# Kernel optimization log

Measured on AMD Instinct MI355X. Metric: run time of the kernel, lower is better.

Reference implementation:

```python
import jax, jax.numpy as jnp
import numpy as np

N_NODES = 10000
N_EDGES = 640000
IN_FEAT = 128
OUT_FEAT = 256


def setup_inputs() -> dict:
    key = jax.random.key(0)
    k_h, k_src, k_dst, k_w, k_b = jax.random.split(key, 5)
    h = jax.random.normal(k_h, (N_NODES, IN_FEAT), dtype=jnp.float32)
    src = jax.random.randint(k_src, (N_EDGES,), 0, N_NODES, dtype=jnp.int64)
    dst = jax.random.randint(k_dst, (N_EDGES,), 0, N_NODES, dtype=jnp.int64)
    W = jax.random.normal(k_w, (2 * IN_FEAT, OUT_FEAT), dtype=jnp.float32) * 0.05
    b = jax.random.normal(k_b, (OUT_FEAT,), dtype=jnp.float32) * 0.05
    return {"h": h, "src": src, "dst": dst, "W": W, "b": b}


def reference(h, src, dst, W, b):
    # Message passing: copy_u('h') then mean-reduce over incoming edges (by dst).
    msgs = h[src]                                   # [E, in_feat] gather
    summed = jax.ops.segment_sum(msgs, dst, num_segments=N_NODES)   # [N, in_feat]
    deg = jax.ops.segment_sum(jnp.ones((src.shape[0],), h.dtype), dst,
                              num_segments=N_NODES)                 # [N]
    h_N = jnp.where(deg[:, None] > 0, summed / jnp.maximum(deg, 1.0)[:, None], 0.0)
    # Concat self + neighbor mean, then dense linear.
    h_total = jnp.concatenate([h, h_N], axis=1)     # [N, 2*in_feat]
    return h_total @ W + b                          # [N, out_feat]
```

## Files before the change

### kernel.cpp

```cpp
#include <hip/hip_runtime.h>
#include <hip/hip_bf16.h>

#define NN 10000
#define NE 640000
#define SB 256
#define EPB 2500
#define NR 625
#define CW 32
#define CE 31
#define CONVB 512

typedef __attribute__((ext_vector_type(8))) short bf16x8;
typedef __attribute__((ext_vector_type(4))) float f32x4;

__device__ __forceinline__ unsigned packbf(float x, float y) {
  __hip_bfloat16 a = __float2bfloat16(x);
  __hip_bfloat16 c = __float2bfloat16(y);
  unsigned short ua = __builtin_bit_cast(unsigned short, a);
  unsigned short uc = __builtin_bit_cast(unsigned short, c);
  return (unsigned)ua | ((unsigned)uc << 16);
}
__device__ __forceinline__ float blo(unsigned u) { return __uint_as_float(u << 16); }
__device__ __forceinline__ float bhi(unsigned u) { return __uint_as_float(u & 0xffff0000u); }

__global__ __launch_bounds__(256) void kA_scatter_conv(
    const float* __restrict__ h, const int* __restrict__ src,
    const int* __restrict__ dst, const float* __restrict__ W,
    unsigned* __restrict__ gbuf, unsigned* __restrict__ hb32,
    unsigned* __restrict__ wb32) {
  int t = threadIdx.x;
  int blk = blockIdx.x;
  if (blk < SB) {
    __shared__ int lc[NR];
    for (int i = t; i < NR; i += 256) lc[i] = 0;
    __syncthreads();
    int base = blk * EPB;
    for (int e = t; e < EPB; e += 256) {
      unsigned d = (unsigned)dst[base + e] & 0x3fffu;
      unsigned sv = (unsigned)src[base + e] & 0x3fffu;
      int range = (int)(d >> 4);
      if (range >= NR) range = NR - 1;
      int r = atomicAdd(&lc[range], 1);
      if (r < CE)
        gbuf[((size_t)range * SB + blk) * CW + 1 + r] = ((d & 15u) << 14) | sv;
    }
    __syncthreads();
    for (int i = t; i < NR; i += 256)
      gbuf[((size_t)i * SB + blk) * CW] = (unsigned)lc[i];
  } else {
    int tid = (blk - SB) * 256 + t;
    const float2* h2 = (const float2*)h;
    for (int j = tid; j < NN * 64; j += CONVB * 256) {
      float2 v = h2[j];
      hb32[j] = packbf(v.x, v.y);
    }
    if (tid < 32768) {
      float2 v = ((const float2*)W)[tid];
      wb32[tid] = packbf(v.x, v.y);
    }
  }
}

__global__ __launch_bounds__(256) void k2_agg_gemm(
    const float* __restrict__ h, const unsigned* __restrict__ gbuf,
    const unsigned* __restrict__ hb32, const unsigned* __restrict__ wb32,
    const float* __restrict__ bias, float* __restrict__ out) {
  __shared__ __align__(16) unsigned short As[16][264];
  __shared__ unsigned short cbuf[16][128];
  __shared__ int lcnt[16];
  int t = threadIdx.x;
  int bm = blockIdx.x;

  if (t < 16) lcnt[t] = 0;

#pragma unroll
  for (int i = 0; i < 2; i++) {
    int q = t + i * 256;
    int row = q >> 5, c4 = q & 31;
    float4 v = *(const float4*)(h + (size_t)(bm * 16 + row) * 128 + c4 * 4);
    uint2 p;
    p.x = packbf(v.x, v.y);
    p.y = packbf(v.z, v.w);
    *(uint2*)(&As[row][c4 * 4]) = p;
  }
  __syncthreads();

  {
    const unsigned* chunk = gbuf + ((size_t)bm * SB + t) * CW;
    int c = (int)(chunk[0] & 0x3fu);
    int kk = c < CE ? c : CE;
    for (int j = 0; j < kk; j++) {
      unsigned v = chunk[1 + j];
      int dstlo = (int)(v >> 14) & 15;
      unsigned sv = v & 0x3fffu;
      int pos = atomicAdd(&lcnt[dstlo], 1);
      if (pos < 128) cbuf[dstlo][pos] = (unsigned short)sv;
    }
  }
  __syncthreads();

  int w = t >> 6, l = t & 63;
#pragma unroll
  for (int i = 0; i < 4; i++) {
    int row = w * 4 + i;
    int deg = lcnt[row];
    int n = deg < 128 ? deg : 128;
    float a0 = 0.f, a1 = 0.f;
    int e = 0;
    for (; e + 7 < n; e += 8) {
      int s0 = cbuf[row][e], s1 = cbuf[row][e + 1], s2 = cbuf[row][e + 2],
          s3 = cbuf[row][e + 3], s4 = cbuf[row][e + 4], s5 = cbuf[row][e + 5],
          s6 = cbuf[row][e + 6], s7 = cbuf[row][e + 7];
      unsigned u0 = hb32[s0 * 64 + l], u1 = hb32[s1 * 64 + l];
      unsigned u2 = hb32[s2 * 64 + l], u3 = hb32[s3 * 64 + l];
      unsigned u4 = hb32[s4 * 64 + l], u5 = hb32[s5 * 64 + l];
      unsigned u6 = hb32[s6 * 64 + l], u7 = hb32[s7 * 64 + l];
      a0 += (blo(u0) + blo(u1)) + (blo(u2) + blo(u3)) +
            ((blo(u4) + blo(u5)) + (blo(u6) + blo(u7)));
      a1 += (bhi(u0) + bhi(u1)) + (bhi(u2) + bhi(u3)) +
            ((bhi(u4) + bhi(u5)) + (bhi(u6) + bhi(u7)));
    }
    for (; e < n; e++) {
      unsigned u = hb32[cbuf[row][e] * 64 + l];
      a0 += blo(u);
      a1 += bhi(u);
    }
    float inv = (deg > 0) ? 1.f / (float)deg : 0.f;
    ((unsigned*)&As[row][128])[l] = packbf(a0 * inv, a1 * inv);
  }
  __syncthreads();

  int lm = l & 15, kb = l >> 4;
  const unsigned short* Wb = (const unsigned short*)wb32;
#pragma unroll
  for (int bn = 0; bn < 4; bn++) {
    int col = bn * 64 + w * 16 + lm;
    bf16x8 bfr[8];
#pragma unroll
    for (int ks = 0; ks < 8; ks++) {
#pragma unroll
      for (int j = 0; j < 8; j++) {
        bfr[ks][j] = (short)Wb[(ks * 32 + kb * 8 + j) * 256 + col];
      }
    }
    f32x4 acc = (f32x4){0.f, 0.f, 0.f, 0.f};
#pragma unroll
    for (int ks = 0; ks < 8; ks++) {
      uint4 araw = *(const uint4*)(&As[lm][ks * 32 + kb * 8]);
      bf16x8 af = __builtin_bit_cast(bf16x8, araw);
      acc = __builtin_amdgcn_mfma_f32_16x16x32_bf16(af, bfr[ks], acc, 0, 0, 0);
    }
    float biasf = bias[col];
#pragma unroll
    for (int reg = 0; reg < 4; reg++) {
      int m = bm * 16 + kb * 4 + reg;
      out[(size_t)m * 256 + col] = acc[reg] + biasf;
    }
  }
}

extern "C" void kernel_launch(void* const* d_in, const int* in_sizes, int n_in,
                              void* d_out, int out_size, void* d_ws, size_t ws_size,
                              hipStream_t stream) {
  const float* h = (const float*)d_in[0];
  const int* src = (const int*)d_in[1];
  const int* dst = (const int*)d_in[2];
  const float* W = (const float*)d_in[3];
  const float* b = (const float*)d_in[4];
  float* out = (float*)d_out;

  char* ws = (char*)d_ws;
  unsigned* gbuf = (unsigned*)(ws + 0);
  unsigned* hb32 = (unsigned*)(ws + 20480000);
  unsigned* wb32 = (unsigned*)(ws + 24674304);

  kA_scatter_conv<<<SB + CONVB, 256, 0, stream>>>(h, src, dst, W, gbuf, hb32, wb32);
  k2_agg_gemm<<<NR, 256, 0, stream>>>(h, gbuf, hb32, wb32, b, out);
}
```

Measured before the change: 106.6 us.

## Prepack W in MFMA fragment order, vectorize neighbor gather, pad edge lists

The scatter kernel now uses 250 blocks of 2560 edges, each thread loading its 10 edges up front, and the h-to-bf16 conversion uses float4 loads. W is prepacked into per-thread MFMA B-fragment order (uint4 per lane), which replaces 64 scalar strided bf16 loads per tile in the GEMM. In the aggregation, each lane gathers 16-byte chunks of neighbor rows, with 4 edge groups per wavefront combined by cross-lane shuffles. Edge lists are padded to a multiple of 8 using a zero row so the loop needs no tail. Self features now come from the precomputed bf16 copy, and the first chunk of gbuf is loaded early as vectors. The costs are more shuffle work and a larger workspace layout with a zero row.

```diff
diff --git a/kernel.cpp b/kernel.cpp
--- a/kernel.cpp
+++ b/kernel.cpp
@@ -3,12 +3,13 @@
 
 #define NN 10000
 #define NE 640000
-#define SB 256
-#define EPB 2500
+#define SB 250
+#define EPB 2560
 #define NR 625
 #define CW 32
 #define CE 31
 #define CONVB 512
+#define ZROW 16000
 
 typedef __attribute__((ext_vector_type(8))) short bf16x8;
 typedef __attribute__((ext_vector_type(4))) float f32x4;
@@ -27,7 +28,7 @@
     const float* __restrict__ h, const int* __restrict__ src,
     const int* __restrict__ dst, const float* __restrict__ W,
     unsigned* __restrict__ gbuf, unsigned* __restrict__ hb32,
-    unsigned* __restrict__ wb32) {
+    uint4* __restrict__ wpk) {
   int t = threadIdx.x;
   int blk = blockIdx.x;
   if (blk < SB) {
@@ -35,120 +36,160 @@
     for (int i = t; i < NR; i += 256) lc[i] = 0;
     __syncthreads();
     int base = blk * EPB;
-    for (int e = t; e < EPB; e += 256) {
-      unsigned d = (unsigned)dst[base + e] & 0x3fffu;
-      unsigned sv = (unsigned)src[base + e] & 0x3fffu;
-      int range = (int)(d >> 4);
+    unsigned dv[10], sv[10];
+#pragma unroll
+    for (int i = 0; i < 10; i++) {
+      int e = base + t + i * 256;
+      dv[i] = (unsigned)dst[e] & 0x3fffu;
+      sv[i] = (unsigned)src[e] & 0x3fffu;
+    }
+#pragma unroll
+    for (int i = 0; i < 10; i++) {
+      int range = (int)(dv[i] >> 4);
       if (range >= NR) range = NR - 1;
       int r = atomicAdd(&lc[range], 1);
       if (r < CE)
-        gbuf[((size_t)range * SB + blk) * CW + 1 + r] = ((d & 15u) << 14) | sv;
+        gbuf[((size_t)range * SB + blk) * CW + 1 + r] = ((dv[i] & 15u) << 14) | sv[i];
     }
     __syncthreads();
     for (int i = t; i < NR; i += 256)
       gbuf[((size_t)i * SB + blk) * CW] = (unsigned)lc[i];
   } else {
     int tid = (blk - SB) * 256 + t;
-    const float2* h2 = (const float2*)h;
-    for (int j = tid; j < NN * 64; j += CONVB * 256) {
-      float2 v = h2[j];
-      hb32[j] = packbf(v.x, v.y);
-    }
-    if (tid < 32768) {
-      float2 v = ((const float2*)W)[tid];
-      wb32[tid] = packbf(v.x, v.y);
+    const float4* h4 = (const float4*)h;
+    for (int j = tid; j < NN * 32; j += CONVB * 256) {
+      float4 v = h4[j];
+      uint2 p;
+      p.x = packbf(v.x, v.y);
+      p.y = packbf(v.z, v.w);
+      *(uint2*)(hb32 + (size_t)j * 2) = p;
+    }
+    if (tid < 64) hb32[(size_t)ZROW * 64 + tid] = 0u;
+    if (tid < 8192) {
+      int tt = tid & 255, bnks = tid >> 8;
+      int ks = bnks & 7, bn = bnks >> 3;
+      int w = tt >> 6, l = tt & 63, kb = l >> 4, lm = l & 15;
+      int col = bn * 64 + w * 16 + lm;
+      int k0 = ks * 32 + kb * 8;
+      uint4 p;
+      p.x = packbf(W[(k0 + 0) * 256 + col], W[(k0 + 1) * 256 + col]);
+      p.y = packbf(W[(k0 + 2) * 256 + col], W[(k0 + 3) * 256 + col]);
+      p.z = packbf(W[(k0 + 4) * 256 + col], W[(k0 + 5) * 256 + col]);
+      p.w = packbf(W[(k0 + 6) * 256 + col], W[(k0 + 7) * 256 + col]);
+      wpk[tid] = p;
     }
   }
 }
 
 __global__ __launch_bounds__(256) void k2_agg_gemm(
-    const float* __restrict__ h, const unsigned* __restrict__ gbuf,
-    const unsigned* __restrict__ hb32, const unsigned* __restrict__ wb32,
-    const float* __restrict__ bias, float* __restrict__ out) {
+    const unsigned* __restrict__ gbuf, const unsigned* __restrict__ hb32,
+    const uint4* __restrict__ wpk, const float* __restrict__ bias,
+    float* __restrict__ out) {
   __shared__ __align__(16) unsigned short As[16][264];
-  __shared__ unsigned short cbuf[16][128];
+  __shared__ __align__(16) unsigned short cbuf[16][128];
   __shared__ int lcnt[16];
+  __shared__ int tdeg[16];
   int t = threadIdx.x;
   int bm = blockIdx.x;
 
+  const unsigned* chunk = gbuf + ((size_t)bm * SB + (t < SB ? t : SB - 1)) * CW;
+  uint4 c0 = *(const uint4*)chunk;
+  uint4 c1 = *(const uint4*)(chunk + 4);
+
   if (t < 16) lcnt[t] = 0;
 
-#pragma unroll
-  for (int i = 0; i < 2; i++) {
-    int q = t + i * 256;
-    int row = q >> 5, c4 = q & 31;
-    float4 v = *(const float4*)(h + (size_t)(bm * 16 + row) * 128 + c4 * 4);
-    uint2 p;
-    p.x = packbf(v.x, v.y);
-    p.y = packbf(v.z, v.w);
-    *(uint2*)(&As[row][c4 * 4]) = p;
-  }
-  __syncthreads();
-
   {
-    const unsigned* chunk = gbuf + ((size_t)bm * SB + t) * CW;
-    int c = (int)(chunk[0] & 0x3fu);
+    int row = t >> 4, c4 = t & 15;
+    uint4 v = *(const uint4*)(hb32 + (size_t)(bm * 16 + row) * 64 + c4 * 4);
+    *(uint4*)(&As[row][c4 * 8]) = v;
+  }
+  __syncthreads();
+
+  if (t < SB) {
+    int c = (int)(c0.x & 0x3fu);
     int kk = c < CE ? c : CE;
-    for (int j = 0; j < kk; j++) {
-      unsigned v = chunk[1 + j];
+    auto route = [&](unsigned v) {
       int dstlo = (int)(v >> 14) & 15;
-      unsigned sv = v & 0x3fffu;
+      unsigned s = v & 0x3fffu;
       int pos = atomicAdd(&lcnt[dstlo], 1);
-      if (pos < 128) cbuf[dstlo][pos] = (unsigned short)sv;
-    }
+      if (pos < 128) cbuf[dstlo][pos] = (unsigned short)s;
+    };
+    if (kk > 0) route(c0.y);
+    if (kk > 1) route(c0.z);
+    if (kk > 2) route(c0.w);
+    if (kk > 3) route(c1.x);
+    if (kk > 4) route(c1.y);
+    if (kk > 5) route(c1.z);
+    if (kk > 6) route(c1.w);
+    for (int j = 7; j < kk; j++) route(chunk[1 + j]);
+  }
+  __syncthreads();
+
+  if (t < 16) {
+    int d = lcnt[t];
+    tdeg[t] = d;
+    int n = d < 128 ? d : 128;
+    int np = (n + 7) & ~7;
+    for (int j = n; j < np; j++) cbuf[t][j] = (unsigned short)ZROW;
+    lcnt[t] = np;
   }
   __syncthreads();
 
   int w = t >> 6, l = t & 63;
+  int g = l >> 4, lm = l & 15;
 #pragma unroll
   for (int i = 0; i < 4; i++) {
     int row = w * 4 + i;
-    int deg = lcnt[row];
-    int n = deg < 128 ? deg : 128;
-    float a0 = 0.f, a1 = 0.f;
-    int e = 0;
-    for (; e + 7 < n; e += 8) {
-      int s0 = cbuf[row][e], s1 = cbuf[row][e + 1], s2 = cbuf[row][e + 2],
-          s3 = cbuf[row][e + 3], s4 = cbuf[row][e + 4], s5 = cbuf[row][e + 5],
-          s6 = cbuf[row][e + 6], s7 = cbuf[row][e + 7];
-      unsigned u0 = hb32[s0 * 64 + l], u1 = hb32[s1 * 64 + l];
-      unsigned u2 = hb32[s2 * 64 + l], u3 = hb32[s3 * 64 + l];
-      unsigned u4 = hb32[s4 * 64 + l], u5 = hb32[s5 * 64 + l];
-      unsigned u6 = hb32[s6 * 64 + l], u7 = hb32[s7 * 64 + l];
-      a0 += (blo(u0) + blo(u1)) + (blo(u2) + blo(u3)) +
-            ((blo(u4) + blo(u5)) + (blo(u6) + blo(u7)));
-      a1 += (bhi(u0) + bhi(u1)) + (bhi(u2) + bhi(u3)) +
-            ((bhi(u4) + bhi(u5)) + (bhi(u6) + bhi(u7)));
-    }
-    for (; e < n; e++) {
-      unsigned u = hb32[cbuf[row][e] * 64 + l];
-      a0 += blo(u);
-      a1 += bhi(u);
-    }
+    int np = lcnt[row];
+    int deg = tdeg[row];
+    float a0 = 0.f, a1 = 0.f, a2 = 0.f, a3 = 0.f;
+    float a4 = 0.f, a5 = 0.f, a6 = 0.f, a7 = 0.f;
+    for (int e = 0; e < np; e += 8) {
+      int s0 = cbuf[row][e + g];
+      int s1 = cbuf[row][e + 4 + g];
+      uint4 u0 = *(const uint4*)(hb32 + (size_t)s0 * 64 + lm * 4);
+      uint4 u1 = *(const uint4*)(hb32 + (size_t)s1 * 64 + lm * 4);
+      a0 += blo(u0.x) + blo(u1.x);
+      a1 += bhi(u0.x) + bhi(u1.x);
+      a2 += blo(u0.y) + blo(u1.y);
+      a3 += bhi(u0.y) + bhi(u1.y);
+      a4 += blo(u0.z) + blo(u1.z);
+      a5 += bhi(u0.z) + bhi(u1.z);
+      a6 += blo(u0.w) + blo(u1.w);
+      a7 += bhi(u0.w) + bhi(u1.w);
+    }
+    a0 += __shfl_xor(a0, 16); a1 += __shfl_xor(a1, 16);
+    a2 += __shfl_xor(a2, 16); a3 += __shfl_xor(a3, 16);
+    a4 += __shfl_xor(a4, 16); a5 += __shfl_xor(a5, 16);
+    a6 += __shfl_xor(a6, 16); a7 += __shfl_xor(a7, 16);
+    a0 += __shfl_xor(a0, 32); a1 += __shfl_xor(a1, 32);
+    a2 += __shfl_xor(a2, 32); a3 += __shfl_xor(a3, 32);
+    a4 += __shfl_xor(a4, 32); a5 += __shfl_xor(a5, 32);
+    a6 += __shfl_xor(a6, 32); a7 += __shfl_xor(a7, 32);
     float inv = (deg > 0) ? 1.f / (float)deg : 0.f;
-    ((unsigned*)&As[row][128])[l] = packbf(a0 * inv, a1 * inv);
-  }
-  __syncthreads();
-
-  int lm = l & 15, kb = l >> 4;
-  const unsigned short* Wb = (const unsigned short*)wb32;
+    if (g == 0) {
+      uint4 p;
+      p.x = packbf(a0 * inv, a1 * inv);
+      p.y = packbf(a2 * inv, a3 * inv);
+      p.z = packbf(a4 * inv, a5 * inv);
+      p.w = packbf(a6 * inv, a7 * inv);
+      *(uint4*)(&As[row][128 + lm * 8]) = p;
+    }
+  }
+  __syncthreads();
+
+  int kb = g;
 #pragma unroll
   for (int bn = 0; bn < 4; bn++) {
     int col = bn * 64 + w * 16 + lm;
-    bf16x8 bfr[8];
+    f32x4 acc = (f32x4){0.f, 0.f, 0.f, 0.f};
 #pragma unroll
     for (int ks = 0; ks < 8; ks++) {
-#pragma unroll
-      for (int j = 0; j < 8; j++) {
-        bfr[ks][j] = (short)Wb[(ks * 32 + kb * 8 + j) * 256 + col];
-      }
-    }
-    f32x4 acc = (f32x4){0.f, 0.f, 0.f, 0.f};
-#pragma unroll
-    for (int ks = 0; ks < 8; ks++) {
+      uint4 braw = wpk[(bn * 8 + ks) * 256 + t];
+      bf16x8 bfr = __builtin_bit_cast(bf16x8, braw);
       uint4 araw = *(const uint4*)(&As[lm][ks * 32 + kb * 8]);
       bf16x8 af = __builtin_bit_cast(bf16x8, araw);
-      acc = __builtin_amdgcn_mfma_f32_16x16x32_bf16(af, bfr[ks], acc, 0, 0, 0);
+      acc = __builtin_amdgcn_mfma_f32_16x16x32_bf16(af, bfr, acc, 0, 0, 0);
     }
     float biasf = bias[col];
 #pragma unroll
@@ -171,9 +212,9 @@
 
   char* ws = (char*)d_ws;
   unsigned* gbuf = (unsigned*)(ws + 0);
-  unsigned* hb32 = (unsigned*)(ws + 20480000);
-  unsigned* wb32 = (unsigned*)(ws + 24674304);
-
-  kA_scatter_conv<<<SB + CONVB, 256, 0, stream>>>(h, src, dst, W, gbuf, hb32, wb32);
-  k2_agg_gemm<<<NR, 256, 0, stream>>>(h, gbuf, hb32, wb32, b, out);
-}
+  unsigned* hb32 = (unsigned*)(ws + 20000000);
+  uint4* wpk = (uint4*)(ws + 24194304);
+
+  kA_scatter_conv<<<SB + CONVB, 256, 0, stream>>>(h, src, dst, W, gbuf, hb32, wpk);
+  k2_agg_gemm<<<NR, 256, 0, stream>>>(gbuf, hb32, wpk, b, out);
+}
```

After: 96.18 us. 1.11x faster.
